# Kernel tuning notes

Measured on AMD Instinct MI355X. Metric: run time of the kernel, lower is better.

The kernel has to match this reference:

```python
import jax, jax.numpy as jnp
import numpy as np

B, S, D = 64, 1024, 256
N_HEADS = 1
HEAD_DIM = D // N_HEADS
MASK_VAL = -10000.0


def setup_inputs() -> dict:
    key = jax.random.key(0)
    k1, k2, k3 = jax.random.split(key, 3)
    x = jax.random.normal(k1, (B, S, D), dtype=jnp.float32)
    W_qkv = jax.random.normal(k2, (D, 3 * D), dtype=jnp.float32) * 0.02
    b_qkv = jnp.zeros((3 * D,), dtype=jnp.float32)
    W_out = jax.random.normal(k3, (D, D), dtype=jnp.float32) * 0.02
    b_out = jnp.zeros((D,), dtype=jnp.float32)
    return {"x": x, "W_qkv": W_qkv, "b_qkv": b_qkv, "W_out": W_out, "b_out": b_out}


def reference(x, W_qkv, b_qkv, W_out, b_out):
    # QKV projection: [B,S,3D]
    qkv = jnp.einsum('bsd,df->bsf', x, W_qkv) + b_qkv
    q, k, v = jnp.split(qkv, 3, axis=2)
    # split heads -> [B,H,S,hd] (H=1)
    def split_heads(t):
        return t.reshape(B, S, N_HEADS, HEAD_DIM).transpose(0, 2, 1, 3)
    q, k, v = split_heads(q), split_heads(k), split_heads(v)
    # scaled scores [B,H,S,S]
    scores = jnp.einsum('bhqd,bhkd->bhqk', q, k) / jnp.sqrt(jnp.float32(HEAD_DIM))
    causal = jnp.tril(jnp.ones((1, 1, S, S), dtype=bool))
    scores = jnp.where(causal, scores, jnp.float32(MASK_VAL))
    attn = jax.nn.softmax(scores, axis=-1)  # dropout deterministic (training=False)
    out = jnp.einsum('bhqk,bhkd->bhqd', attn, v)
    # merge heads -> [B,S,D]
    out = out.transpose(0, 2, 1, 3).reshape(B, S, D)
    out = jnp.einsum('bsd,de->bse', out, W_out) + b_out
    return out, attn
```

## Files before the change

### kernel.cpp

```cpp
#include <hip/hip_runtime.h>
#include <hip/hip_bf16.h>

#define BB 64
#define SS 1024
#define DDIM 256

typedef unsigned short u16;
typedef __attribute__((ext_vector_type(4))) float f4;
typedef __attribute__((ext_vector_type(8))) short bf16x8;
typedef __attribute__((ext_vector_type(4))) short bf16x4;
typedef __attribute__((ext_vector_type(4))) float f32x4;

__device__ inline u16 f2b(float f) {
  unsigned int u = __float_as_uint(f);
  unsigned int r = (u + 0x7fffu + ((u >> 16) & 1u)) >> 16;
  return (u16)r;
}

#define GLOAD16(g, l)                                                  \
  __builtin_amdgcn_global_load_lds(                                    \
      (const __attribute__((address_space(1))) void*)(g),              \
      (__attribute__((address_space(3))) void*)(l), 16, 0, 0)

__global__ __launch_bounds__(256) void cast_x(const float* __restrict__ x,
                                              u16* __restrict__ xb, int n8) {
  int i = blockIdx.x * 256 + threadIdx.x;
  const int stride = gridDim.x * 256;
  for (; i < n8; i += stride) {
    f4 a = ((const f4*)x)[2 * i];
    f4 b = ((const f4*)x)[2 * i + 1];
    bf16x8 o;
    o[0] = f2b(a[0]); o[1] = f2b(a[1]); o[2] = f2b(a[2]); o[3] = f2b(a[3]);
    o[4] = f2b(b[0]); o[5] = f2b(b[1]); o[6] = f2b(b[2]); o[7] = f2b(b[3]);
    ((bf16x8*)xb)[i] = o;
  }
}

__global__ __launch_bounds__(256) void cast_w(const float* __restrict__ Wqkv,
                                              const float* __restrict__ Wout,
                                              u16* __restrict__ Wqkvt,
                                              u16* __restrict__ Woutt) {
  int t = blockIdx.x * 256 + threadIdx.x;
  if (t < 256 * 768) {
    int k = t / 768, n = t % 768;
    Wqkvt[n * 256 + k] = f2b(Wqkv[t]);
  }
  if (t < 256 * 256) {
    int k = t / 256, n = t % 256;
    Woutt[n * 256 + k] = f2b(Wout[t]);
  }
}

template <int EPI, int NXT>
__global__ __launch_bounds__(256) void gemm_mfma(
    const u16* __restrict__ A, const u16* __restrict__ Bt,
    const float* __restrict__ bias, float* __restrict__ outF,
    u16* __restrict__ Qb, u16* __restrict__ Kb, u16* __restrict__ Vt) {
  __shared__ u16 As[128 * 64];
  __shared__ u16 Bs[128 * 64];
  const int t = threadIdx.x;
  const int w = t >> 6, l = t & 63;
  const int lr = l & 15, lg = l >> 4;
  const int id = blockIdx.x;
  const int r8 = id & 7;
  const int tt = id >> 3;
  const int xt = tt % NXT;
  const int yt = (tt / NXT) * 8 + r8;
  const int m0 = yt * 128, n0 = xt * 128;
  const int wm = (w >> 1) * 64, wn = (w & 1) * 64;

  f32x4 acc[4][4] = {};

  for (int k0 = 0; k0 < 256; k0 += 64) {
    __syncthreads();
#pragma unroll
    for (int j = 0; j < 4; ++j) {
      int idx = t + j * 256;
      int row = idx >> 3, c = idx & 7;
      f4 va = *(const f4*)&A[(size_t)(m0 + row) * 256 + k0 + c * 8];
      *(f4*)&As[row * 64 + ((c ^ (row & 7)) * 8)] = va;
      f4 vb = *(const f4*)&Bt[(size_t)(n0 + row) * 256 + k0 + c * 8];
      *(f4*)&Bs[row * 64 + ((c ^ (row & 7)) * 8)] = vb;
    }
    __syncthreads();
#pragma unroll
    for (int kc = 0; kc < 2; ++kc) {
      bf16x8 af[4], bfr[4];
#pragma unroll
      for (int f = 0; f < 4; ++f) {
        int ar = wm + f * 16 + lr;
        af[f] = *(const bf16x8*)&As[ar * 64 + (((kc * 4 + lg) ^ (ar & 7)) * 8)];
        int br = wn + f * 16 + lr;
        bfr[f] = *(const bf16x8*)&Bs[br * 64 + (((kc * 4 + lg) ^ (br & 7)) * 8)];
      }
#pragma unroll
      for (int i = 0; i < 4; ++i)
#pragma unroll
        for (int jn = 0; jn < 4; ++jn)
          acc[i][jn] = __builtin_amdgcn_mfma_f32_16x16x32_bf16(
              af[i], bfr[jn], acc[i][jn], 0, 0, 0);
    }
  }

#pragma unroll
  for (int i = 0; i < 4; ++i) {
    const int mbase = m0 + wm + i * 16 + lg * 4;
#pragma unroll
    for (int jn = 0; jn < 4; ++jn) {
      const int n = n0 + wn + jn * 16 + lr;
      const float bv = bias[n];
      if (EPI == 0) {
#pragma unroll
        for (int r = 0; r < 4; ++r)
          outF[(size_t)(mbase + r) * 256 + n] = acc[i][jn][r] + bv;
      } else {
        if (n < 256) {
#pragma unroll
          for (int r = 0; r < 4; ++r)
            Qb[(size_t)(mbase + r) * 256 + n] = f2b(acc[i][jn][r] + bv);
        } else if (n < 512) {
#pragma unroll
          for (int r = 0; r < 4; ++r)
            Kb[(size_t)(mbase + r) * 256 + (n - 256)] = f2b(acc[i][jn][r] + bv);
        } else {
          const int d = n - 512;
          const int b = mbase >> 10, sl = mbase & 1023;
          bf16x4 pk;
#pragma unroll
          for (int r = 0; r < 4; ++r) pk[r] = f2b(acc[i][jn][r] + bv);
          *(bf16x4*)&Vt[((size_t)b * 256 + d) * 1024 + sl] = pk;
        }
      }
    }
  }
}

__global__ __launch_bounds__(256) void attn_fused(
    const u16* __restrict__ Qg, const u16* __restrict__ Kg,
    const u16* __restrict__ Vtg, float* __restrict__ attn,
    u16* __restrict__ outa) {
  __shared__ u16 pool[35328];
  u16* Ks = pool;
  u16* Vs = pool + 16384;
  u16* Ps = pool + 32768;

  const int t = threadIdx.x;
  const int w = t >> 6, l = t & 63;
  const int lr = l & 15, lg = l >> 4;
  const int id = blockIdx.x;
  const int b = (id & 7) * 8 + ((id >> 3) & 7);
  const int pair = id >> 6;
  const int qta = pair, qtb = 15 - pair;
  const int d0w = w * 64;

  const u16* Kbase = Kg + (size_t)b * SS * DDIM;
  const u16* Vbase = Vtg + (size_t)b * DDIM * SS;

  auto stageK = [&](int kt, int buf) {
    const int rbase = 8 * w;
#pragma unroll
    for (int i = 0; i < 4; ++i) {
      const int rr = rbase + 2 * i + (l >> 5);
      const int chunk = l & 31;
      const int csrc = (chunk & 24) | ((chunk & 7) ^ (rr & 7));
      const u16* g = Kbase + (size_t)(kt * 32 + rr) * DDIM + csrc * 8;
      GLOAD16(g, Ks + buf * 8192 + (rbase + 2 * i) * 256);
    }
  };
  auto stageV = [&](int kt, int buf) {
    const int dbase = 64 * w;
#pragma unroll
    for (int i = 0; i < 4; ++i) {
      const int dd = dbase + 16 * i + (l >> 2);
      const u16* g = Vbase + (size_t)dd * SS + kt * 32 + (l & 3) * 8;
      GLOAD16(g, Vs + buf * 8192 + (dbase + 16 * i) * 32);
    }
  };
  auto loadQ = [&](int qt, bf16x8* qf) {
    const u16* qb = Qg + ((size_t)(b * SS + qt * 64 + w * 16 + lr)) * DDIM;
#pragma unroll
    for (int kc = 0; kc < 8; ++kc)
      qf[kc] = *(const bf16x8*)&qb[kc * 32 + lg * 8];
  };

  bf16x8 qfA[8], qfB[8];
  loadQ(qta, qfA);
  loadQ(qtb, qfB);
  const int lastA = 2 * qta + 1, lastB = 2 * qtb + 1;
  float raA[4] = {0.f, 0.f, 0.f, 0.f}, raB[4] = {0.f, 0.f, 0.f, 0.f};

  stageK(0, 0);
  __syncthreads();
  for (int kt = 0; kt <= lastB; ++kt) {
    const int buf = kt & 1;
    if (kt < lastB) stageK(kt + 1, buf ^ 1);
    const bool doA = (kt <= lastA);
#pragma unroll
    for (int sf = 0; sf < 2; ++sf) {
      const int srow = sf * 16 + lr;
      const u16* kr = Ks + buf * 8192 + srow * 256;
      f32x4 sA = {0.f, 0.f, 0.f, 0.f}, sB = {0.f, 0.f, 0.f, 0.f};
#pragma unroll
      for (int kc = 0; kc < 8; ++kc) {
        const int c = kc * 4 + lg;
        const int ch = (c & 24) | ((c & 7) ^ (srow & 7));
        bf16x8 bfr = *(const bf16x8*)&kr[ch * 8];
        sB = __builtin_amdgcn_mfma_f32_16x16x32_bf16(qfB[kc], bfr, sB, 0, 0, 0);
        if (doA)
          sA = __builtin_amdgcn_mfma_f32_16x16x32_bf16(qfA[kc], bfr, sA, 0, 0, 0);
      }
      const int scol = kt * 32 + srow - lr + lr;
      {
        const int qrow = qtb * 64 + w * 16 + lg * 4;
#pragma unroll
        for (int r = 0; r < 4; ++r)
          raB[r] += (scol <= qrow + r) ? __expf(sB[r] * 0.0625f) : 0.f;
      }
      if (doA) {
        const int qrow = qta * 64 + w * 16 + lg * 4;
#pragma unroll
        for (int r = 0; r < 4; ++r)
          raA[r] += (scol <= qrow + r) ? __expf(sA[r] * 0.0625f) : 0.f;
      }
    }
    __syncthreads();
  }
#pragma unroll
  for (int m = 1; m < 16; m <<= 1) {
#pragma unroll
    for (int r = 0; r < 4; ++r) {
      raA[r] += __shfl_xor(raA[r], m, 64);
      raB[r] += __shfl_xor(raB[r], m, 64);
    }
  }
  float invA[4], invB[4];
#pragma unroll
  for (int r = 0; r < 4; ++r) {
    invA[r] = 1.0f / raA[r];
    invB[r] = 1.0f / raB[r];
  }

  for (int tile = 0; tile < 2; ++tile) {
    const int qt = tile ? qtb : qta;
    const int last = 2 * qt + 1;
    bf16x8 qf[8];
    loadQ(qt, qf);
    float inv[4];
#pragma unroll
    for (int r = 0; r < 4; ++r) inv[r] = tile ? invB[r] : invA[r];
    f32x4 oacc[4][4];
#pragma unroll
    for (int qb = 0; qb < 4; ++qb)
#pragma unroll
      for (int df = 0; df < 4; ++df) oacc[qb][df] = (f32x4){0.f, 0.f, 0.f, 0.f};

    float* attnw = attn + ((size_t)(b * SS + qt * 64 + w * 16)) * SS;

    __syncthreads();
    stageK(0, 0);
    stageV(0, 0);
    __syncthreads();

    for (int kt = 0; kt <= last; ++kt) {
      const int buf = kt & 1;
#pragma unroll
      for (int sf = 0; sf < 2; ++sf) {
        const int srow = sf * 16 + lr;
        const u16* kr = Ks + buf * 8192 + srow * 256;
        f32x4 s = {0.f, 0.f, 0.f, 0.f};
#pragma unroll
        for (int kc = 0; kc < 8; ++kc) {
          const int c = kc * 4 + lg;
          const int ch = (c & 24) | ((c & 7) ^ (srow & 7));
          bf16x8 bfr = *(const bf16x8*)&kr[ch * 8];
          s = __builtin_amdgcn_mfma_f32_16x16x32_bf16(qf[kc], bfr, s, 0, 0, 0);
        }
        const int scol = kt * 32 + sf * 16 + lr;
        const int qrow = qt * 64 + w * 16 + lg * 4;
#pragma unroll
        for (int r = 0; r < 4; ++r) {
          const float e = (scol <= qrow + r) ? __expf(s[r] * 0.0625f) : 0.f;
          Ps[(w * 16 + lg * 4 + r) * 40 + sf * 16 + lr] = f2b(e * inv[r]);
        }
      }
#pragma unroll
      for (int g2 = 0; g2 < 2; ++g2) {
        const int row = g2 * 8 + (l >> 3);
        const int col = (l & 7) * 4;
        bf16x4 pv = *(const bf16x4*)&Ps[(w * 16 + row) * 40 + col];
        f4 o;
#pragma unroll
        for (int j = 0; j < 4; ++j)
          o[j] = __uint_as_float(((unsigned)(u16)pv[j]) << 16);
        *(f4*)&attnw[(size_t)row * SS + kt * 32 + col] = o;
      }
      __syncthreads();
      if (kt < last) {
        stageK(kt + 1, buf ^ 1);
        stageV(kt + 1, buf ^ 1);
      }
      bf16x8 vfr[4];
      const u16* vb = Vs + buf * 8192;
#pragma unroll
      for (int df = 0; df < 4; ++df)
        vfr[df] = *(const bf16x8*)&vb[(d0w + df * 16 + lr) * 32 + lg * 8];
#pragma unroll
      for (int qb = 0; qb < 4; ++qb) {
        bf16x8 pa = *(const bf16x8*)&Ps[(qb * 16 + lr) * 40 + lg * 8];
#pragma unroll
        for (int df = 0; df < 4; ++df)
          oacc[qb][df] = __builtin_amdgcn_mfma_f32_16x16x32_bf16(
              pa, vfr[df], oacc[qb][df], 0, 0, 0);
      }
      __syncthreads();
    }

    {
      const f4 z = {0.f, 0.f, 0.f, 0.f};
      for (int c0 = (qt + 1) * 64; c0 < SS; c0 += 32) {
#pragma unroll
        for (int g2 = 0; g2 < 2; ++g2) {
          const int row = g2 * 8 + (l >> 3);
          *(f4*)&attnw[(size_t)row * SS + c0 + (l & 7) * 4] = z;
        }
      }
    }

#pragma unroll
    for (int qb = 0; qb < 4; ++qb)
#pragma unroll
      for (int df = 0; df < 4; ++df)
#pragma unroll
        for (int r = 0; r < 4; ++r)
          pool[(qb * 16 + lg * 4 + r) * 264 + d0w + df * 16 + lr] =
              f2b(oacc[qb][df][r]);
    __syncthreads();
    {
      const size_t obase = (size_t)(b * SS + qt * 64);
#pragma unroll
      for (int i = 0; i < 8; ++i) {
        const int row = w * 16 + 2 * i + (l >> 5);
        bf16x8 v = *(const bf16x8*)&pool[row * 264 + (l & 31) * 8];
        *(bf16x8*)&outa[(obase + row) * DDIM + (l & 31) * 8] = v;
      }
    }
  }
}

extern "C" void kernel_launch(void* const* d_in, const int* in_sizes, int n_in,
                              void* d_out, int out_size, void* d_ws,
                              size_t ws_size, hipStream_t stream) {
  const float* x    = (const float*)d_in[0];
  const float* Wqkv = (const float*)d_in[1];
  const float* bqkv = (const float*)d_in[2];
  const float* Wout = (const float*)d_in[3];
  const float* bout = (const float*)d_in[4];

  float* out  = (float*)d_out;
  float* attn = out + (size_t)BB * SS * DDIM;

  const size_t NTOK = (size_t)BB * SS;
  u16* ws = (u16*)d_ws;
  u16* xb    = ws;
  u16* Qb    = xb + NTOK * DDIM;
  u16* Kb    = Qb + NTOK * DDIM;
  u16* Vt    = Kb + NTOK * DDIM;
  u16* outa  = Vt + NTOK * DDIM;
  u16* Wqkvt = outa + NTOK * DDIM;
  u16* Woutt = Wqkvt + 768 * 256;

  cast_x<<<2048, 256, 0, stream>>>(x, xb, (int)(NTOK * DDIM / 8));
  cast_w<<<768, 256, 0, stream>>>(Wqkv, Wout, Wqkvt, Woutt);

  gemm_mfma<1, 6><<<3072, 256, 0, stream>>>(xb, Wqkvt, bqkv, nullptr, Qb, Kb,
                                            Vt);
  attn_fused<<<512, 256, 0, stream>>>(Qb, Kb, Vt, attn, outa);
  gemm_mfma<0, 2><<<1024, 256, 0, stream>>>(outa, Woutt, bout, out, nullptr,
                                            nullptr, nullptr);
}
```

Baseline: 256.2 us.

## Async LDS loads in QKV GEMM; per-wave PV ownership with earlier K/V prefetch

The QKV GEMM tile staging now uses global_load_lds direct-to-LDS copies instead of going through registers. In the attention pass, each wave now computes PV for its own 16 query rows across all 256 head dims. Because a wave reads only the P rows it wrote, one barrier per key tile goes away, and the prefetch of the next K/V tile is issued at the start of the iteration. This aims to overlap global loads with the QK and softmax work and to cut synchronisation, at the cost of more V fragment reads from LDS per wave and more accumulator registers.

Result: slower. 272.4 us (+6.3%).

```diff
diff --git a/kernel.cpp b/kernel.cpp
--- a/kernel.cpp
+++ b/kernel.cpp
@@ -71,16 +71,18 @@
 
   f32x4 acc[4][4] = {};
 
+  const int srow = w * 8 + (l >> 3);
+  const int csrc = (l & 7) ^ (srow & 7);
+
   for (int k0 = 0; k0 < 256; k0 += 64) {
     __syncthreads();
 #pragma unroll
-    for (int j = 0; j < 4; ++j) {
-      int idx = t + j * 256;
-      int row = idx >> 3, c = idx & 7;
-      f4 va = *(const f4*)&A[(size_t)(m0 + row) * 256 + k0 + c * 8];
-      *(f4*)&As[row * 64 + ((c ^ (row & 7)) * 8)] = va;
-      f4 vb = *(const f4*)&Bt[(size_t)(n0 + row) * 256 + k0 + c * 8];
-      *(f4*)&Bs[row * 64 + ((c ^ (row & 7)) * 8)] = vb;
+    for (int i = 0; i < 4; ++i) {
+      const int row = i * 32 + srow;
+      GLOAD16(&A[(size_t)(m0 + row) * 256 + k0 + csrc * 8],
+              &As[(i * 32 + w * 8) * 64]);
+      GLOAD16(&Bt[(size_t)(n0 + row) * 256 + k0 + csrc * 8],
+              &Bs[(i * 32 + w * 8) * 64]);
     }
     __syncthreads();
 #pragma unroll
@@ -151,7 +153,6 @@
   const int b = (id & 7) * 8 + ((id >> 3) & 7);
   const int pair = id >> 6;
   const int qta = pair, qtb = 15 - pair;
-  const int d0w = w * 64;
 
   const u16* Kbase = Kg + (size_t)b * SS * DDIM;
   const u16* Vbase = Vtg + (size_t)b * DDIM * SS;
@@ -169,12 +170,11 @@
   };
   auto stageV = [&](int kt, int buf) {
     const int dbase = 64 * w;
-#pragma unroll
-    for (int i = 0; i < 4; ++i) {
-      const int dd = dbase + 16 * i + (l >> 2);
-      const u16* g = Vbase + (size_t)dd * SS + kt * 32 + (l & 3) * 8;
-      GLOAD16(g, Vs + buf * 8192 + (dbase + 16 * i) * 32);
-    }
+    const int dd = dbase + (l >> 2);
+    const u16* g0 = Vbase + (size_t)dd * SS + kt * 32 + (l & 3) * 8;
+#pragma unroll
+    for (int i = 0; i < 4; ++i)
+      GLOAD16(g0 + (size_t)16 * i * SS, Vs + buf * 8192 + (dbase + 16 * i) * 32);
   };
   auto loadQ = [&](int qt, bf16x8* qf) {
     const u16* qb = Qg + ((size_t)(b * SS + qt * 64 + w * 16 + lr)) * DDIM;
@@ -209,7 +209,7 @@
         if (doA)
           sA = __builtin_amdgcn_mfma_f32_16x16x32_bf16(qfA[kc], bfr, sA, 0, 0, 0);
       }
-      const int scol = kt * 32 + srow - lr + lr;
+      const int scol = kt * 32 + sf * 16 + lr;
       {
         const int qrow = qtb * 64 + w * 16 + lg * 4;
 #pragma unroll
@@ -248,11 +248,9 @@
     float inv[4];
 #pragma unroll
     for (int r = 0; r < 4; ++r) inv[r] = tile ? invB[r] : invA[r];
-    f32x4 oacc[4][4];
-#pragma unroll
-    for (int qb = 0; qb < 4; ++qb)
-#pragma unroll
-      for (int df = 0; df < 4; ++df) oacc[qb][df] = (f32x4){0.f, 0.f, 0.f, 0.f};
+    f32x4 oacc[16];
+#pragma unroll
+    for (int df = 0; df < 16; ++df) oacc[df] = (f32x4){0.f, 0.f, 0.f, 0.f};
 
     float* attnw = attn + ((size_t)(b * SS + qt * 64 + w * 16)) * SS;
 
@@ -263,6 +261,10 @@
 
     for (int kt = 0; kt <= last; ++kt) {
       const int buf = kt & 1;
+      if (kt < last) {
+        stageK(kt + 1, buf ^ 1);
+        stageV(kt + 1, buf ^ 1);
+      }
 #pragma unroll
       for (int sf = 0; sf < 2; ++sf) {
         const int srow = sf * 16 + lr;
@@ -294,23 +296,15 @@
           o[j] = __uint_as_float(((unsigned)(u16)pv[j]) << 16);
         *(f4*)&attnw[(size_t)row * SS + kt * 32 + col] = o;
       }
-      __syncthreads();
-      if (kt < last) {
-        stageK(kt + 1, buf ^ 1);
-        stageV(kt + 1, buf ^ 1);
-      }
-      bf16x8 vfr[4];
-      const u16* vb = Vs + buf * 8192;
-#pragma unroll
-      for (int df = 0; df < 4; ++df)
-        vfr[df] = *(const bf16x8*)&vb[(d0w + df * 16 + lr) * 32 + lg * 8];
-#pragma unroll
-      for (int qb = 0; qb < 4; ++qb) {
-        bf16x8 pa = *(const bf16x8*)&Ps[(qb * 16 + lr) * 40 + lg * 8];
-#pragma unroll
-        for (int df = 0; df < 4; ++df)
-          oacc[qb][df] = __builtin_amdgcn_mfma_f32_16x16x32_bf16(
-              pa, vfr[df], oacc[qb][df], 0, 0, 0);
+      {
+        bf16x8 pa = *(const bf16x8*)&Ps[(w * 16 + lr) * 40 + lg * 8];
+        const u16* vb = Vs + buf * 8192;
+#pragma unroll
+        for (int df = 0; df < 16; ++df) {
+          bf16x8 vfr = *(const bf16x8*)&vb[(df * 16 + lr) * 32 + lg * 8];
+          oacc[df] = __builtin_amdgcn_mfma_f32_16x16x32_bf16(pa, vfr, oacc[df],
+                                                            0, 0, 0);
+        }
       }
       __syncthreads();
     }
@@ -326,15 +320,12 @@
       }
     }
 
-#pragma unroll
-    for (int qb = 0; qb < 4; ++qb)
-#pragma unroll
-      for (int df = 0; df < 4; ++df)
-#pragma unroll
-        for (int r = 0; r < 4; ++r)
-          pool[(qb * 16 + lg * 4 + r) * 264 + d0w + df * 16 + lr] =
-              f2b(oacc[qb][df][r]);
-    __syncthreads();
+    __syncthreads();
+#pragma unroll
+    for (int df = 0; df < 16; ++df)
+#pragma unroll
+      for (int r = 0; r < 4; ++r)
+        pool[(w * 16 + lg * 4 + r) * 264 + df * 16 + lr] = f2b(oacc[df][r]);
     {
       const size_t obase = (size_t)(b * SS + qt * 64);
 #pragma unroll
```
